# Kernel optimization log

Measured on AMD Instinct MI355X. Metric: run time of the kernel, lower is better.

## Reference

```python
import jax, jax.numpy as jnp
import numpy as np

B, N, M, DIM, H, DH = 2, 2048, 2048, 512, 8, 64
INNER = H * DH
SCALE = DH ** -0.5  # cosine_sim=False default
EPS = 1e-5


def layer_norm(x, g, b):
    mu = x.mean(-1, keepdims=True)
    var = ((x - mu) ** 2).mean(-1, keepdims=True)
    return (x - mu) * jax.lax.rsqrt(var + EPS) * g + b


def setup_inputs() -> dict:
    key = jax.random.key(0)
    ks = jax.random.split(key, 8)
    x = jax.random.normal(ks[0], (B, N, DIM), dtype=jnp.float32)
    context = jax.random.normal(ks[1], (B, M, DIM), dtype=jnp.float32)
    mask = jax.random.randint(ks[2], (B, M), 0, 2).astype(bool)
    Wq = jax.random.normal(ks[3], (DIM, INNER), dtype=jnp.float32) * 0.02
    Wkv = jax.random.normal(ks[4], (DIM, 2 * INNER), dtype=jnp.float32) * 0.02
    Wo = jax.random.normal(ks[5], (INNER, DIM), dtype=jnp.float32) * 0.02
    ln_g = jnp.ones((DIM,), jnp.float32)
    ln_b = jnp.zeros((DIM,), jnp.float32)
    lno_g = jnp.ones((DIM,), jnp.float32)
    lno_b = jnp.zeros((DIM,), jnp.float32)
    return {"x": x, "context": context, "mask": mask, "ln_g": ln_g, "ln_b": ln_b,
            "Wq": Wq, "Wkv": Wkv, "Wo": Wo, "lno_g": lno_g, "lno_b": lno_b}


def reference(x, context, mask, ln_g, ln_b, Wq, Wkv, Wo, lno_g, lno_b):
    b, n, _ = x.shape
    xn = layer_norm(x, ln_g, ln_b)
    ctx = context  # norm_context=False -> Identity
    q = (xn @ Wq).reshape(b, n, H, DH).transpose(0, 2, 1, 3)          # b h n d
    kv = ctx @ Wkv
    k, v = jnp.split(kv, 2, axis=-1)
    k = k.reshape(b, -1, H, DH).transpose(0, 2, 1, 3)                 # b h m d
    v = v.reshape(b, -1, H, DH).transpose(0, 2, 1, 3)
    q = q * SCALE
    k = k * SCALE
    sim = jnp.einsum('bhid,bhjd->bhij', q, k)                         # b h n m (256 MB)
    max_neg = -jnp.finfo(sim.dtype).max
    sim = jnp.where(mask[:, None, None, :], sim, max_neg)
    attn = jax.nn.softmax(sim.astype(jnp.float32), axis=-1).astype(sim.dtype)
    out = jnp.einsum('bhij,bhjd->bhid', attn, v)
    out = out.transpose(0, 2, 1, 3).reshape(b, n, INNER)
    return layer_norm(out @ Wo, lno_g, lno_b)
```

## Files before the change

### kernel.cpp

```cpp
#include <hip/hip_runtime.h>
#include <stdint.h>

typedef float f32x4 __attribute__((ext_vector_type(4)));
typedef float f32x16 __attribute__((ext_vector_type(16)));
typedef __bf16 bf16x8 __attribute__((ext_vector_type(8)));
typedef unsigned int uint2v __attribute__((ext_vector_type(2)));

#define MFMA16(a,b,c) __builtin_amdgcn_mfma_f32_16x16x32_bf16((a),(b),(c),0,0,0)
#define MFMA32(a,b,c) __builtin_amdgcn_mfma_f32_32x32x16_bf16((a),(b),(c),0,0,0)

__device__ __forceinline__ unsigned short f2bf(float f){
  unsigned int u = __float_as_uint(f);
  u += 0x7FFFu + ((u >> 16) & 1u);
  return (unsigned short)(u >> 16);
}

__device__ __forceinline__ unsigned cvtpk(float lo, float hi){
  unsigned r;
  asm volatile("v_cvt_pk_bf16_f32 %0, %1, %2" : "=v"(r) : "v"(lo), "v"(hi));
  return r;
}

__device__ __forceinline__ float fexp2(float x){
#if __has_builtin(__builtin_amdgcn_exp2f)
  return __builtin_amdgcn_exp2f(x);
#else
  return exp2f(x);
#endif
}

__device__ __forceinline__ void plswap(unsigned &a, unsigned &b){
#if __has_builtin(__builtin_amdgcn_permlane32_swap)
  uint2v r = __builtin_amdgcn_permlane32_swap(a, b, false, false);
  a = r[0]; b = r[1];
#else
  unsigned xa = __shfl_xor(a, 32), xb = __shfl_xor(b, 32);
  int hi = (threadIdx.x & 63) >> 5;
  unsigned na = hi ? xb : a;
  unsigned nb = hi ? b : xa;
  a = na; b = nb;
#endif
}

__device__ __forceinline__ float xpair_max(float x){
  unsigned a = __float_as_uint(x), b = a;
  plswap(a, b);
  return fmaxf(__uint_as_float(a), __uint_as_float(b));
}
__device__ __forceinline__ float xpair_sum(float x){
  unsigned a = __float_as_uint(x), b = a;
  plswap(a, b);
  return __uint_as_float(a) + __uint_as_float(b);
}

__device__ __forceinline__ void stage16(const unsigned short* g, unsigned short* l){
  __builtin_amdgcn_global_load_lds(
      (const __attribute__((address_space(1))) void*)g,
      (__attribute__((address_space(3))) void*)l, 16, 0, 0);
}

__global__ __launch_bounds__(256) void k_prep(
    const float* __restrict__ Wq, const float* __restrict__ Wkv, const float* __restrict__ Wo,
    const float* __restrict__ x, const float* __restrict__ ln_g, const float* __restrict__ ln_b,
    const float* __restrict__ ctx, const int* __restrict__ mask,
    unsigned short* __restrict__ WqT, unsigned short* __restrict__ WkvT, unsigned short* __restrict__ WoT,
    unsigned short* __restrict__ xn, unsigned short* __restrict__ cb, unsigned int* __restrict__ mb)
{
  __shared__ float tile[32][33];
  const int bid = blockIdx.x, t = threadIdx.x;
  if (bid < 1024) {
    const float* W; unsigned short* WT; int N, bx, by;
    if (bid < 256)      { W = Wq;  WT = WqT;  N = 512;  bx = bid & 15;        by = bid >> 4; }
    else if (bid < 768) { W = Wkv; WT = WkvT; N = 1024; bx = (bid-256) & 31;  by = (bid-256) >> 5; }
    else                { W = Wo;  WT = WoT;  N = 512;  bx = (bid-768) & 15;  by = (bid-768) >> 4; }
    const int tx = t & 31, ty = t >> 5;
    #pragma unroll
    for (int i = 0; i < 4; i++)
      tile[ty + i*8][tx] = W[(size_t)(by*32 + ty + i*8) * N + bx*32 + tx];
    __syncthreads();
    #pragma unroll
    for (int i = 0; i < 4; i++)
      WT[(size_t)(bx*32 + ty + i*8) * 512 + by*32 + tx] = f2bf(tile[tx][ty + i*8]);
  } else if (bid < 2048) {
    int row = (bid - 1024) * 4 + (t >> 6);
    int lane = t & 63;
    const float4* xr = (const float4*)(x + (size_t)row * 512);
    float4 a = xr[lane], c = xr[64 + lane];
    float s = a.x + a.y + a.z + a.w + c.x + c.y + c.z + c.w;
    #pragma unroll
    for (int o = 32; o; o >>= 1) s += __shfl_xor(s, o);
    float mu = s * (1.0f / 512.0f);
    float va = (a.x-mu)*(a.x-mu) + (a.y-mu)*(a.y-mu) + (a.z-mu)*(a.z-mu) + (a.w-mu)*(a.w-mu)
             + (c.x-mu)*(c.x-mu) + (c.y-mu)*(c.y-mu) + (c.z-mu)*(c.z-mu) + (c.w-mu)*(c.w-mu);
    #pragma unroll
    for (int o = 32; o; o >>= 1) va += __shfl_xor(va, o);
    float inv = rsqrtf(va * (1.0f / 512.0f) + 1e-5f);
    const float4* gp = (const float4*)ln_g;
    const float4* bp = (const float4*)ln_b;
    float4 g0 = gp[lane], g1 = gp[64 + lane], b0 = bp[lane], b1 = bp[64 + lane];
    ushort4* op = (ushort4*)(xn + (size_t)row * 512);
    op[lane]      = make_ushort4(f2bf((a.x-mu)*inv*g0.x + b0.x), f2bf((a.y-mu)*inv*g0.y + b0.y),
                                 f2bf((a.z-mu)*inv*g0.z + b0.z), f2bf((a.w-mu)*inv*g0.w + b0.w));
    op[64 + lane] = make_ushort4(f2bf((c.x-mu)*inv*g1.x + b1.x), f2bf((c.y-mu)*inv*g1.y + b1.y),
                                 f2bf((c.z-mu)*inv*g1.z + b1.z), f2bf((c.w-mu)*inv*g1.w + b1.w));
  } else if (bid < 4096) {
    int i = (bid - 2048) * 256 + t;
    float4 v = ((const float4*)ctx)[i];
    ((ushort4*)cb)[i] = make_ushort4(f2bf(v.x), f2bf(v.y), f2bf(v.z), f2bf(v.w));
  } else {
    int g = (bid - 4096) * 4 + (t >> 6);
    int ln = t & 63;
    int v = mask[g * 64 + ln];
    unsigned long long bb = __ballot(v != 0);
    if (ln == 0) { mb[g*2] = (unsigned)bb; mb[g*2+1] = (unsigned)(bb >> 32); }
  }
}

__global__ __launch_bounds__(256) void k_layernorm_f(
    const float* __restrict__ X, const float* __restrict__ G,
    const float* __restrict__ Bt, float* __restrict__ out)
{
  int row = blockIdx.x * 4 + (threadIdx.x >> 6);
  int lane = threadIdx.x & 63;
  const float4* xr = (const float4*)(X + (size_t)row * 512);
  float4 a = xr[lane], c = xr[64 + lane];
  float s = a.x + a.y + a.z + a.w + c.x + c.y + c.z + c.w;
  #pragma unroll
  for (int o = 32; o; o >>= 1) s += __shfl_xor(s, o);
  float mu = s * (1.0f / 512.0f);
  float va = (a.x-mu)*(a.x-mu) + (a.y-mu)*(a.y-mu) + (a.z-mu)*(a.z-mu) + (a.w-mu)*(a.w-mu)
           + (c.x-mu)*(c.x-mu) + (c.y-mu)*(c.y-mu) + (c.z-mu)*(c.z-mu) + (c.w-mu)*(c.w-mu);
  #pragma unroll
  for (int o = 32; o; o >>= 1) va += __shfl_xor(va, o);
  float inv = rsqrtf(va * (1.0f / 512.0f) + 1e-5f);
  const float4* gp = (const float4*)G;
  const float4* bp = (const float4*)Bt;
  float4 g0 = gp[lane], g1 = gp[64 + lane], b0 = bp[lane], b1 = bp[64 + lane];
  float4 y0, y1;
  y0.x = (a.x-mu)*inv*g0.x + b0.x; y0.y = (a.y-mu)*inv*g0.y + b0.y;
  y0.z = (a.z-mu)*inv*g0.z + b0.z; y0.w = (a.w-mu)*inv*g0.w + b0.w;
  y1.x = (c.x-mu)*inv*g1.x + b1.x; y1.y = (c.y-mu)*inv*g1.y + b1.y;
  y1.z = (c.z-mu)*inv*g1.z + b1.z; y1.w = (c.w-mu)*inv*g1.w + b1.w;
  float4* op = (float4*)(out + (size_t)row * 512);
  op[lane] = y0; op[64 + lane] = y1;
}

template<int MODE>
__device__ __forceinline__ void gemm_body(
    const unsigned short* __restrict__ A, const unsigned short* __restrict__ BT,
    void* __restrict__ out0, void* __restrict__ out1, int bx, int by,
    unsigned short* smem)
{
  unsigned short* As = smem;
  unsigned short* Bs = smem + 2*64*64;
  const int t = threadIdx.x;
  const int lane = t & 63, l16 = lane & 15, lhi = lane >> 4;
  const int w = t >> 6, wm = w >> 1, wn = w & 1;
  const int rowBase = by * 64;
  const int colBase = bx * 128;
  const int srr = lane >> 3, scw = lane & 7;

  f32x4 acc[2][4];
  #pragma unroll
  for (int i = 0; i < 2; i++)
    #pragma unroll
    for (int j = 0; j < 4; j++)
      acc[i][j] = f32x4{0.f, 0.f, 0.f, 0.f};

  auto STAGE = [&](int buf, int kt) {
    unsigned short* Ab = As + buf * 4096;
    unsigned short* Bb = Bs + buf * 8192;
    #pragma unroll
    for (int i = 0; i < 2; i++) {
      int rr = i * 32 + w * 8 + srr;
      stage16(A + (size_t)(rowBase + rr) * 512 + kt * 64 + ((scw ^ (rr & 7)) * 8),
              Ab + (i * 32 + w * 8) * 64);
    }
    #pragma unroll
    for (int i = 0; i < 4; i++) {
      int rr = i * 32 + w * 8 + srr;
      stage16(BT + (size_t)(colBase + rr) * 512 + kt * 64 + ((scw ^ (rr & 7)) * 8),
              Bb + (i * 32 + w * 8) * 64);
    }
  };

  STAGE(0, 0);
  __syncthreads();
  for (int kt = 0; kt < 8; ++kt) {
    const int buf = kt & 1;
    if (kt < 7) STAGE(buf ^ 1, kt + 1);
    const char* Ab = (const char*)(As + buf * 4096);
    const char* Bb = (const char*)(Bs + buf * 8192);
    #pragma unroll
    for (int ks = 0; ks < 2; ++ks) {
      bf16x8 af[2], bb[4];
      #pragma unroll
      for (int mi = 0; mi < 2; mi++) {
        int rr = wm * 32 + mi * 16 + l16;
        int cc = ks * 4 + lhi;
        af[mi] = *(const bf16x8*)(Ab + rr * 128 + ((cc ^ (rr & 7)) * 16));
      }
      #pragma unroll
      for (int ni = 0; ni < 4; ni++) {
        int rr = wn * 64 + ni * 16 + l16;
        int cc = ks * 4 + lhi;
        bb[ni] = *(const bf16x8*)(Bb + rr * 128 + ((cc ^ (rr & 7)) * 16));
      }
      #pragma unroll
      for (int mi = 0; mi < 2; mi++)
        #pragma unroll
        for (int ni = 0; ni < 4; ni++)
          acc[mi][ni] = MFMA16(af[mi], bb[ni], acc[mi][ni]);
    }
    __syncthreads();
  }

  if constexpr (MODE == 2) {
    const int r0 = rowBase + wm * 32 + lhi * 4;
    const int c0 = colBase + wn * 64 + l16;
    #pragma unroll
    for (int mi = 0; mi < 2; mi++)
      #pragma unroll
      for (int ni = 0; ni < 4; ni++)
        #pragma unroll
        for (int r = 0; r < 4; r++)
          ((float*)out0)[(size_t)(r0 + mi * 16 + r) * 512 + c0 + ni * 16] = acc[mi][ni][r];
  } else {
    unsigned short* stg = smem;
    const bool isV = (MODE == 1) && (colBase >= 512);
    if (!isV) {
      #pragma unroll
      for (int mi = 0; mi < 2; mi++) {
        int rl = wm * 32 + mi * 16 + lhi * 4;
        int tl = rl >> 5;
        #pragma unroll
        for (int ni = 0; ni < 4; ni++) {
          int cl = wn * 64 + ni * 16 + l16;
          int hl = cl >> 6, d = cl & 63;
          int rbase = (hl * 2 + tl) * 2048 + (d >> 4) * 512 + 256 * ((d >> 3) & 1) + (d & 7);
          #pragma unroll
          for (int r = 0; r < 4; r++)
            stg[rbase + ((rl + r) & 31) * 8] = f2bf(acc[mi][ni][r]);
        }
      }
    } else {
      #pragma unroll
      for (int mi = 0; mi < 2; mi++) {
        int rl = wm * 32 + mi * 16 + lhi * 4;
        int tl = rl >> 5, kvr = rl & 31;
        #pragma unroll
        for (int ni = 0; ni < 4; ni++) {
          int cl = wn * 64 + ni * 16 + l16;
          int hl = cl >> 6, d = cl & 63;
          int off = (hl * 2 + tl) * 2048 + (d >> 5) * 1024 + ((kvr >> 4) & 1) * 512
                  + ((d & 31) + 32 * ((kvr >> 3) & 1)) * 8 + (kvr & 7);
          ushort4 p = make_ushort4(f2bf(acc[mi][ni][0]), f2bf(acc[mi][ni][1]),
                                   f2bf(acc[mi][ni][2]), f2bf(acc[mi][ni][3]));
          *(ushort4*)(stg + off) = p;
        }
      }
    }
    __syncthreads();
    const int bb2 = rowBase >> 11;
    const int hh0 = (colBase & 511) >> 6;
    const int tile0 = (rowBase & 2047) >> 5;
    unsigned short* gout = (unsigned short*)(isV ? out1 : out0);
    #pragma unroll
    for (int ridx = 0; ridx < 4; ridx++) {
      int hl = ridx >> 1, tl = ridx & 1;
      size_t gb = ((size_t)((bb2 * 8 + hh0 + hl) * 64 + tile0 + tl)) * 2048 + t * 8;
      *(uint4*)(gout + gb) = *(const uint4*)(stg + ridx * 2048 + t * 8);
    }
  }
}

__global__ __launch_bounds__(256, 2) void k_qkv(
    const unsigned short* __restrict__ xn, const unsigned short* __restrict__ WqT,
    unsigned short* __restrict__ Qp,
    const unsigned short* __restrict__ cb, const unsigned short* __restrict__ WkvT,
    unsigned short* __restrict__ Kp, unsigned short* __restrict__ Vp)
{
  __shared__ __align__(16) unsigned short smem[2*64*64 + 2*128*64];
  const int bid = blockIdx.x;
  const int xcd = bid & 7, loc = bid >> 3;
  const int mloc = loc / 12, ct = loc % 12;
  const int mtile = xcd * 8 + mloc;
  if (ct < 4) gemm_body<0>(xn, WqT, Qp, nullptr, ct, mtile, smem);
  else        gemm_body<1>(cb, WkvT, Kp, Vp, ct - 4, mtile, smem);
}

__global__ __launch_bounds__(256, 2) void k_oproj(
    const unsigned short* __restrict__ ao, const unsigned short* __restrict__ WoT,
    float* __restrict__ proj)
{
  __shared__ __align__(16) unsigned short smem[2*64*64 + 2*128*64];
  const int bid = blockIdx.x;
  const int xcd = bid & 7, loc = bid >> 3;
  const int mloc = loc >> 2, ct = loc & 3;
  const int mtile = xcd * 8 + mloc;
  gemm_body<2>(ao, WoT, proj, nullptr, ct, mtile, smem);
}

__global__ __launch_bounds__(256, 3) void k_attn(
    const unsigned short* __restrict__ Qp, const unsigned short* __restrict__ Kp,
    const unsigned short* __restrict__ Vp, const unsigned int* __restrict__ mb,
    unsigned short* __restrict__ O)
{
  __shared__ __align__(16) float mbuf[3][64][34];
  const int t = threadIdx.x, lane = t & 63, q5 = lane & 31, hi = lane >> 5;
  const int w = t >> 6;
  const int bid = blockIdx.x;
  const int bh = (bid & 7) * 2 + (bid >> 9);
  const int qt = (bid >> 3) & 63;
  const int q0 = qt * 32;
  const int b = bh >> 3, h = bh & 7;
  const float C2f = 0.022542110013890053f;

  bf16x8 qf[4];
  {
    const unsigned short* qp = Qp + (size_t)(bh * 64 + qt) * 2048 + lane * 8;
    #pragma unroll
    for (int kk = 0; kk < 4; kk++) qf[kk] = *(const bf16x8*)(qp + kk * 512);
  }
  const unsigned short* kpb = Kp + (size_t)bh * 131072 + lane * 8;
  const unsigned short* vpb = Vp + (size_t)bh * 131072 + lane * 8;
  const unsigned int* mbp = mb + b * 64;

  float mrun = -3e38f, lrun = 0.f;
  f32x16 acc0, acc1;
  #pragma unroll
  for (int i = 0; i < 16; i++) { acc0[i] = 0.f; acc1[i] = 0.f; }

  bf16x8 kf[4], vf[4];
  auto loadK = [&](int tile) {
    #pragma unroll
    for (int kk = 0; kk < 4; kk++)
      kf[kk] = *(const bf16x8*)(kpb + (size_t)tile * 2048 + kk * 512);
  };
  auto loadV = [&](int tile) {
    #pragma unroll
    for (int i = 0; i < 4; i++)
      vf[i] = *(const bf16x8*)(vpb + (size_t)tile * 2048 + i * 512);
  };

  const int tb = w * 16;
  loadK(tb); loadV(tb);
  for (int it = 0; it < 16; ++it) {
    const int ti = tb + it;

    f32x16 s;
    #pragma unroll
    for (int i = 0; i < 16; i++) s[i] = 0.f;
    __builtin_amdgcn_s_setprio(1);
    #pragma unroll
    for (int kk = 0; kk < 4; kk++) s = MFMA32(kf[kk], qf[kk], s);
    __builtin_amdgcn_s_setprio(0);
    if (it < 15) loadK(ti + 1);

    float m0 = fmaxf(fmaxf(s[0], s[1]),  fmaxf(s[2], s[3]));
    float m1 = fmaxf(fmaxf(s[4], s[5]),  fmaxf(s[6], s[7]));
    float m2 = fmaxf(fmaxf(s[8], s[9]),  fmaxf(s[10], s[11]));
    float m3 = fmaxf(fmaxf(s[12], s[13]), fmaxf(s[14], s[15]));
    float tmax = fmaxf(fmaxf(m0, m1), fmaxf(m2, m3));
    tmax = xpair_max(tmax);
    if (!__all(tmax <= mrun + 400.f)) {
      float mnew = fmaxf(mrun, tmax);
      float sf = fexp2((mrun - mnew) * C2f);
      lrun *= sf;
      #pragma unroll
      for (int i = 0; i < 16; i++) { acc0[i] *= sf; acc1[i] *= sf; }
      mrun = mnew;
    }
    unsigned mh = mbp[ti] >> (hi * 4);
    float nb = -mrun * C2f;
    float p[16];
    #pragma unroll
    for (int r = 0; r < 16; r++) {
      float pv = fexp2(fmaf(s[r], C2f, nb));
      p[r] = ((mh >> ((r & 3) + 8 * (r >> 2))) & 1u) ? pv : 0.f;
    }
    float rsa = (p[0] + p[1]) + (p[2] + p[3]);
    float rsb = (p[4] + p[5]) + (p[6] + p[7]);
    float rsc = (p[8] + p[9]) + (p[10] + p[11]);
    float rsd = (p[12] + p[13]) + (p[14] + p[15]);
    lrun += (rsa + rsb) + (rsc + rsd);

    unsigned wd[8];
    #pragma unroll
    for (int i = 0; i < 8; i++) wd[i] = cvtpk(p[2 * i], p[2 * i + 1]);
    plswap(wd[0], wd[2]); plswap(wd[1], wd[3]);
    plswap(wd[4], wd[6]); plswap(wd[5], wd[7]);
    union { unsigned u[4]; bf16x8 v; } U0, U1;
    U0.u[0] = wd[0]; U0.u[1] = wd[1]; U0.u[2] = wd[2]; U0.u[3] = wd[3];
    U1.u[0] = wd[4]; U1.u[1] = wd[5]; U1.u[2] = wd[6]; U1.u[3] = wd[7];

    __builtin_amdgcn_s_setprio(1);
    acc0 = MFMA32(vf[0], U0.v, acc0);
    acc0 = MFMA32(vf[1], U1.v, acc0);
    acc1 = MFMA32(vf[2], U0.v, acc1);
    acc1 = MFMA32(vf[3], U1.v, acc1);
    __builtin_amdgcn_s_setprio(0);
    if (it < 15) loadV(ti + 1);
  }

  if (w) {
    #pragma unroll
    for (int i = 0; i < 16; i++) { mbuf[w-1][lane][i] = acc0[i]; mbuf[w-1][lane][16 + i] = acc1[i]; }
    mbuf[w-1][lane][32] = mrun; mbuf[w-1][lane][33] = lrun;
  }
  __syncthreads();
  if (!w) {
    float mo[3], lo[3];
    #pragma unroll
    for (int wv = 0; wv < 3; wv++) { mo[wv] = mbuf[wv][lane][32]; lo[wv] = mbuf[wv][lane][33]; }
    float mN = fmaxf(fmaxf(mrun, mo[0]), fmaxf(mo[1], mo[2]));
    float sf0 = fexp2((mrun - mN) * C2f);
    float sfv[3];
    float lsum = lrun * sf0;
    #pragma unroll
    for (int wv = 0; wv < 3; wv++) { sfv[wv] = fexp2((mo[wv] - mN) * C2f); lsum += lo[wv] * sfv[wv]; }
    lsum = xpair_sum(lsum);
    float linv = 1.f / lsum;
    float a2[32];
    #pragma unroll
    for (int i = 0; i < 16; i++) {
      float v0 = acc0[i] * sf0, v1 = acc1[i] * sf0;
      #pragma unroll
      for (int wv = 0; wv < 3; wv++) {
        v0 += mbuf[wv][lane][i] * sfv[wv];
        v1 += mbuf[wv][lane][16 + i] * sfv[wv];
      }
      a2[i] = v0 * linv;
      a2[16 + i] = v1 * linv;
    }
    unsigned short* ot = (unsigned short*)&mbuf[0][0][0];
    #pragma unroll
    for (int d2 = 0; d2 < 2; d2++)
      #pragma unroll
      for (int i = 0; i < 8; i++) {
        int d0 = ((2 * i) & 3) + 8 * (i >> 1) + 4 * hi + 32 * d2;
        unsigned wv2 = cvtpk(a2[d2 * 16 + 2 * i], a2[d2 * 16 + 2 * i + 1]);
        *(unsigned*)(ot + q5 * 72 + d0) = wv2;
      }
    #pragma unroll
    for (int it2 = 0; it2 < 4; ++it2) {
      int row = (lane >> 3) + it2 * 8, ch = lane & 7;
      uint4 val = *(const uint4*)(ot + row * 72 + ch * 8);
      *(uint4*)(O + ((size_t)(b * 2048 + q0 + row)) * 512 + h * 64 + ch * 8) = val;
    }
  }
}

extern "C" void kernel_launch(void* const* d_in, const int* in_sizes, int n_in,
                              void* d_out, int out_size, void* d_ws, size_t ws_size,
                              hipStream_t stream) {
  const float* x     = (const float*)d_in[0];
  const float* ctx   = (const float*)d_in[1];
  const int*   mask  = (const int*)d_in[2];
  const float* ln_g  = (const float*)d_in[3];
  const float* ln_b  = (const float*)d_in[4];
  const float* Wq    = (const float*)d_in[5];
  const float* Wkv   = (const float*)d_in[6];
  const float* Wo    = (const float*)d_in[7];
  const float* lno_g = (const float*)d_in[8];
  const float* lno_b = (const float*)d_in[9];
  float* out = (float*)d_out;

  char* ws = (char*)d_ws;
  unsigned short* WqT  = (unsigned short*)(ws + 0);
  unsigned short* WkvT = (unsigned short*)(ws + (size_t)1 * (1 << 19));
  unsigned short* WoT  = (unsigned short*)(ws + (size_t)3 * (1 << 19));
  unsigned short* xn   = (unsigned short*)(ws + (size_t)2  * (1 << 20));
  unsigned short* cb   = (unsigned short*)(ws + (size_t)6  * (1 << 20));
  unsigned short* Qp   = (unsigned short*)(ws + (size_t)10 * (1 << 20));
  unsigned short* Kp   = (unsigned short*)(ws + (size_t)14 * (1 << 20));
  unsigned short* Vp   = (unsigned short*)(ws + (size_t)18 * (1 << 20));
  unsigned short* ao   = (unsigned short*)(ws + (size_t)22 * (1 << 20));
  float* proj          = (float*)(ws + (size_t)26 * (1 << 20));
  unsigned int* mbw    = (unsigned int*)(ws + (size_t)26 * (1 << 20));

  k_prep<<<4112, 256, 0, stream>>>(Wq, Wkv, Wo, x, ln_g, ln_b, ctx, mask,
                                   WqT, WkvT, WoT, xn, cb, mbw);
  k_qkv<<<768, 256, 0, stream>>>(xn, WqT, Qp, cb, WkvT, Kp, Vp);
  k_attn<<<1024, 256, 0, stream>>>(Qp, Kp, Vp, mbw, ao);
  k_oproj<<<256, 256, 0, stream>>>(ao, WoT, proj);
  k_layernorm_f<<<1024, 256, 0, stream>>>(proj, lno_g, lno_b, out);
}
```

Measured before the change: 63.23 us.

## Process two query tiles per attention block to reuse K/V fragment loads

Each attention block now handles two 32-row query tiles that share every K and V fragment loaded per iteration, which halves global K/V traffic per query and halves the grid to 512 blocks. Launch bounds drop from 3 to 2 blocks per SM because of the doubled accumulators and Q registers. The cost is lower occupancy, less latency hiding, and a second merge pass with extra barriers at the end.

```diff
diff --git a/kernel.cpp b/kernel.cpp
--- a/kernel.cpp
+++ b/kernel.cpp
@@ -301,7 +301,7 @@
   gemm_body<2>(ao, WoT, proj, nullptr, ct, mtile, smem);
 }
 
-__global__ __launch_bounds__(256, 3) void k_attn(
+__global__ __launch_bounds__(256, 2) void k_attn(
     const unsigned short* __restrict__ Qp, const unsigned short* __restrict__ Kp,
     const unsigned short* __restrict__ Vp, const unsigned int* __restrict__ mb,
     unsigned short* __restrict__ O)
@@ -310,26 +310,29 @@
   const int t = threadIdx.x, lane = t & 63, q5 = lane & 31, hi = lane >> 5;
   const int w = t >> 6;
   const int bid = blockIdx.x;
-  const int bh = (bid & 7) * 2 + (bid >> 9);
-  const int qt = (bid >> 3) & 63;
-  const int q0 = qt * 32;
+  const int bh = (bid & 7) * 2 + (bid >> 8);
+  const int g = (bid >> 3) & 31;
+  const int qtA = g * 2, qtB = g * 2 + 1;
   const int b = bh >> 3, h = bh & 7;
   const float C2f = 0.022542110013890053f;
 
-  bf16x8 qf[4];
+  bf16x8 qfA[4], qfB[4];
   {
-    const unsigned short* qp = Qp + (size_t)(bh * 64 + qt) * 2048 + lane * 8;
-    #pragma unroll
-    for (int kk = 0; kk < 4; kk++) qf[kk] = *(const bf16x8*)(qp + kk * 512);
+    const unsigned short* qpA = Qp + (size_t)(bh * 64 + qtA) * 2048 + lane * 8;
+    const unsigned short* qpB = Qp + (size_t)(bh * 64 + qtB) * 2048 + lane * 8;
+    #pragma unroll
+    for (int kk = 0; kk < 4; kk++) { qfA[kk] = *(const bf16x8*)(qpA + kk * 512);
+                                     qfB[kk] = *(const bf16x8*)(qpB + kk * 512); }
   }
   const unsigned short* kpb = Kp + (size_t)bh * 131072 + lane * 8;
   const unsigned short* vpb = Vp + (size_t)bh * 131072 + lane * 8;
   const unsigned int* mbp = mb + b * 64;
 
-  float mrun = -3e38f, lrun = 0.f;
-  f32x16 acc0, acc1;
+  float mrunA = -3e38f, lrunA = 0.f;
+  float mrunB = -3e38f, lrunB = 0.f;
+  f32x16 accA0, accA1, accB0, accB1;
   #pragma unroll
-  for (int i = 0; i < 16; i++) { acc0[i] = 0.f; acc1[i] = 0.f; }
+  for (int i = 0; i < 16; i++) { accA0[i] = 0.f; accA1[i] = 0.f; accB0[i] = 0.f; accB1[i] = 0.f; }
 
   bf16x8 kf[4], vf[4];
   auto loadK = [&](int tile) {
@@ -343,24 +346,12 @@
       vf[i] = *(const bf16x8*)(vpb + (size_t)tile * 2048 + i * 512);
   };
 
-  const int tb = w * 16;
-  loadK(tb); loadV(tb);
-  for (int it = 0; it < 16; ++it) {
-    const int ti = tb + it;
-
-    f32x16 s;
-    #pragma unroll
-    for (int i = 0; i < 16; i++) s[i] = 0.f;
-    __builtin_amdgcn_s_setprio(1);
-    #pragma unroll
-    for (int kk = 0; kk < 4; kk++) s = MFMA32(kf[kk], qf[kk], s);
-    __builtin_amdgcn_s_setprio(0);
-    if (it < 15) loadK(ti + 1);
-
-    float m0 = fmaxf(fmaxf(s[0], s[1]),  fmaxf(s[2], s[3]));
-    float m1 = fmaxf(fmaxf(s[4], s[5]),  fmaxf(s[6], s[7]));
-    float m2 = fmaxf(fmaxf(s[8], s[9]),  fmaxf(s[10], s[11]));
-    float m3 = fmaxf(fmaxf(s[12], s[13]), fmaxf(s[14], s[15]));
+  auto smax_pv = [&](f32x16& sX, float& mrun, float& lrun, f32x16& a0, f32x16& a1,
+                     unsigned mh) {
+    float m0 = fmaxf(fmaxf(sX[0], sX[1]),  fmaxf(sX[2], sX[3]));
+    float m1 = fmaxf(fmaxf(sX[4], sX[5]),  fmaxf(sX[6], sX[7]));
+    float m2 = fmaxf(fmaxf(sX[8], sX[9]),  fmaxf(sX[10], sX[11]));
+    float m3 = fmaxf(fmaxf(sX[12], sX[13]), fmaxf(sX[14], sX[15]));
     float tmax = fmaxf(fmaxf(m0, m1), fmaxf(m2, m3));
     tmax = xpair_max(tmax);
     if (!__all(tmax <= mrun + 400.f)) {
@@ -368,15 +359,14 @@
       float sf = fexp2((mrun - mnew) * C2f);
       lrun *= sf;
       #pragma unroll
-      for (int i = 0; i < 16; i++) { acc0[i] *= sf; acc1[i] *= sf; }
+      for (int i = 0; i < 16; i++) { a0[i] *= sf; a1[i] *= sf; }
       mrun = mnew;
     }
-    unsigned mh = mbp[ti] >> (hi * 4);
     float nb = -mrun * C2f;
     float p[16];
     #pragma unroll
     for (int r = 0; r < 16; r++) {
-      float pv = fexp2(fmaf(s[r], C2f, nb));
+      float pv = fexp2(fmaf(sX[r], C2f, nb));
       p[r] = ((mh >> ((r & 3) + 8 * (r >> 2))) & 1u) ? pv : 0.f;
     }
     float rsa = (p[0] + p[1]) + (p[2] + p[3]);
@@ -395,60 +385,86 @@
     U1.u[0] = wd[4]; U1.u[1] = wd[5]; U1.u[2] = wd[6]; U1.u[3] = wd[7];
 
     __builtin_amdgcn_s_setprio(1);
-    acc0 = MFMA32(vf[0], U0.v, acc0);
-    acc0 = MFMA32(vf[1], U1.v, acc0);
-    acc1 = MFMA32(vf[2], U0.v, acc1);
-    acc1 = MFMA32(vf[3], U1.v, acc1);
+    a0 = MFMA32(vf[0], U0.v, a0);
+    a0 = MFMA32(vf[1], U1.v, a0);
+    a1 = MFMA32(vf[2], U0.v, a1);
+    a1 = MFMA32(vf[3], U1.v, a1);
     __builtin_amdgcn_s_setprio(0);
+  };
+
+  const int tb = w * 16;
+  loadK(tb); loadV(tb);
+  for (int it = 0; it < 16; ++it) {
+    const int ti = tb + it;
+
+    f32x16 sA, sB;
+    #pragma unroll
+    for (int i = 0; i < 16; i++) { sA[i] = 0.f; sB[i] = 0.f; }
+    __builtin_amdgcn_s_setprio(1);
+    #pragma unroll
+    for (int kk = 0; kk < 4; kk++) sA = MFMA32(kf[kk], qfA[kk], sA);
+    #pragma unroll
+    for (int kk = 0; kk < 4; kk++) sB = MFMA32(kf[kk], qfB[kk], sB);
+    __builtin_amdgcn_s_setprio(0);
+    if (it < 15) loadK(ti + 1);
+
+    unsigned mh = mbp[ti] >> (hi * 4);
+    smax_pv(sA, mrunA, lrunA, accA0, accA1, mh);
+    smax_pv(sB, mrunB, lrunB, accB0, accB1, mh);
     if (it < 15) loadV(ti + 1);
   }
 
-  if (w) {
-    #pragma unroll
-    for (int i = 0; i < 16; i++) { mbuf[w-1][lane][i] = acc0[i]; mbuf[w-1][lane][16 + i] = acc1[i]; }
-    mbuf[w-1][lane][32] = mrun; mbuf[w-1][lane][33] = lrun;
-  }
-  __syncthreads();
-  if (!w) {
-    float mo[3], lo[3];
-    #pragma unroll
-    for (int wv = 0; wv < 3; wv++) { mo[wv] = mbuf[wv][lane][32]; lo[wv] = mbuf[wv][lane][33]; }
-    float mN = fmaxf(fmaxf(mrun, mo[0]), fmaxf(mo[1], mo[2]));
-    float sf0 = fexp2((mrun - mN) * C2f);
-    float sfv[3];
-    float lsum = lrun * sf0;
-    #pragma unroll
-    for (int wv = 0; wv < 3; wv++) { sfv[wv] = fexp2((mo[wv] - mN) * C2f); lsum += lo[wv] * sfv[wv]; }
-    lsum = xpair_sum(lsum);
-    float linv = 1.f / lsum;
-    float a2[32];
-    #pragma unroll
-    for (int i = 0; i < 16; i++) {
-      float v0 = acc0[i] * sf0, v1 = acc1[i] * sf0;
-      #pragma unroll
-      for (int wv = 0; wv < 3; wv++) {
-        v0 += mbuf[wv][lane][i] * sfv[wv];
-        v1 += mbuf[wv][lane][16 + i] * sfv[wv];
+  auto merge_write = [&](f32x16& a0, f32x16& a1, float mr, float lr, int qt) {
+    if (w) {
+      #pragma unroll
+      for (int i = 0; i < 16; i++) { mbuf[w-1][lane][i] = a0[i]; mbuf[w-1][lane][16 + i] = a1[i]; }
+      mbuf[w-1][lane][32] = mr; mbuf[w-1][lane][33] = lr;
+    }
+    __syncthreads();
+    if (!w) {
+      float mo[3], lo[3];
+      #pragma unroll
+      for (int wv = 0; wv < 3; wv++) { mo[wv] = mbuf[wv][lane][32]; lo[wv] = mbuf[wv][lane][33]; }
+      float mN = fmaxf(fmaxf(mr, mo[0]), fmaxf(mo[1], mo[2]));
+      float sf0 = fexp2((mr - mN) * C2f);
+      float sfv[3];
+      float lsum = lr * sf0;
+      #pragma unroll
+      for (int wv = 0; wv < 3; wv++) { sfv[wv] = fexp2((mo[wv] - mN) * C2f); lsum += lo[wv] * sfv[wv]; }
+      lsum = xpair_sum(lsum);
+      float linv = 1.f / lsum;
+      float a2[32];
+      #pragma unroll
+      for (int i = 0; i < 16; i++) {
+        float v0 = a0[i] * sf0, v1 = a1[i] * sf0;
+        #pragma unroll
+        for (int wv = 0; wv < 3; wv++) {
+          v0 += mbuf[wv][lane][i] * sfv[wv];
+          v1 += mbuf[wv][lane][16 + i] * sfv[wv];
+        }
+        a2[i] = v0 * linv;
+        a2[16 + i] = v1 * linv;
       }
-      a2[i] = v0 * linv;
-      a2[16 + i] = v1 * linv;
-    }
-    unsigned short* ot = (unsigned short*)&mbuf[0][0][0];
-    #pragma unroll
-    for (int d2 = 0; d2 < 2; d2++)
-      #pragma unroll
-      for (int i = 0; i < 8; i++) {
-        int d0 = ((2 * i) & 3) + 8 * (i >> 1) + 4 * hi + 32 * d2;
-        unsigned wv2 = cvtpk(a2[d2 * 16 + 2 * i], a2[d2 * 16 + 2 * i + 1]);
-        *(unsigned*)(ot + q5 * 72 + d0) = wv2;
+      unsigned short* ot = (unsigned short*)&mbuf[0][0][0];
+      #pragma unroll
+      for (int d2 = 0; d2 < 2; d2++)
+        #pragma unroll
+        for (int i = 0; i < 8; i++) {
+          int d0 = ((2 * i) & 3) + 8 * (i >> 1) + 4 * hi + 32 * d2;
+          unsigned wv2 = cvtpk(a2[d2 * 16 + 2 * i], a2[d2 * 16 + 2 * i + 1]);
+          *(unsigned*)(ot + q5 * 72 + d0) = wv2;
+        }
+      #pragma unroll
+      for (int it2 = 0; it2 < 4; ++it2) {
+        int row = (lane >> 3) + it2 * 8, ch = lane & 7;
+        uint4 val = *(const uint4*)(ot + row * 72 + ch * 8);
+        *(uint4*)(O + ((size_t)(b * 2048 + qt * 32 + row)) * 512 + h * 64 + ch * 8) = val;
       }
-    #pragma unroll
-    for (int it2 = 0; it2 < 4; ++it2) {
-      int row = (lane >> 3) + it2 * 8, ch = lane & 7;
-      uint4 val = *(const uint4*)(ot + row * 72 + ch * 8);
-      *(uint4*)(O + ((size_t)(b * 2048 + q0 + row)) * 512 + h * 64 + ch * 8) = val;
-    }
-  }
+    }
+    __syncthreads();
+  };
+  merge_write(accA0, accA1, mrunA, lrunA, qtA);
+  merge_write(accB0, accB1, mrunB, lrunB, qtB);
 }
 
 extern "C" void kernel_launch(void* const* d_in, const int* in_sizes, int n_in,
@@ -482,7 +498,7 @@
   k_prep<<<4112, 256, 0, stream>>>(Wq, Wkv, Wo, x, ln_g, ln_b, ctx, mask,
                                    WqT, WkvT, WoT, xn, cb, mbw);
   k_qkv<<<768, 256, 0, stream>>>(xn, WqT, Qp, cb, WkvT, Kp, Vp);
-  k_attn<<<1024, 256, 0, stream>>>(Qp, Kp, Vp, mbw, ao);
+  k_attn<<<512, 256, 0, stream>>>(Qp, Kp, Vp, mbw, ao);
   k_oproj<<<256, 256, 0, stream>>>(ao, WoT, proj);
   k_layernorm_f<<<1024, 256, 0, stream>>>(proj, lno_g, lno_b, out);
 }
```

Measured after the change: 61.68 us. -2.4%, faster.

## Fold key mask into an MFMA bias and pair two KV tiles per iteration

Applied to the files above, without the earlier changes.

The key mask becomes an additive bf16 bias tensor in k_prep. It is applied by one extra MFMA per KV tile, using a one-hot Q fragment, instead of per-element bit tests and selects after exp. Each attention block now covers two query tiles, with two waves per query tile splitting the keys. Each wave handles two KV tiles per loop iteration, which doubles registers and the work per wave, while the grid is halved and launch bounds drop to 2. The intent is to remove mask ALU work and shrink the cross-wave merge, at the cost of fewer resident waves for latency hiding and higher register pressure.

```diff
diff --git a/kernel.cpp b/kernel.cpp
--- a/kernel.cpp
+++ b/kernel.cpp
@@ -64,7 +64,7 @@
     const float* __restrict__ x, const float* __restrict__ ln_g, const float* __restrict__ ln_b,
     const float* __restrict__ ctx, const int* __restrict__ mask,
     unsigned short* __restrict__ WqT, unsigned short* __restrict__ WkvT, unsigned short* __restrict__ WoT,
-    unsigned short* __restrict__ xn, unsigned short* __restrict__ cb, unsigned int* __restrict__ mb)
+    unsigned short* __restrict__ xn, unsigned short* __restrict__ cb, unsigned short* __restrict__ kbias)
 {
   __shared__ float tile[32][33];
   const int bid = blockIdx.x, t = threadIdx.x;
@@ -108,11 +108,16 @@
     float4 v = ((const float4*)ctx)[i];
     ((ushort4*)cb)[i] = make_ushort4(f2bf(v.x), f2bf(v.y), f2bf(v.z), f2bf(v.w));
   } else {
-    int g = (bid - 4096) * 4 + (t >> 6);
-    int ln = t & 63;
-    int v = mask[g * 64 + ln];
-    unsigned long long bb = __ballot(v != 0);
-    if (ln == 0) { mb[g*2] = (unsigned)bb; mb[g*2+1] = (unsigned)(bb >> 32); }
+    int i = (bid - 4096) * 256 + t;
+    int b2 = i >> 11, kv = i & 2047;
+    int tl = kv >> 5, ln = kv & 31;
+    unsigned short bias = (mask[b2 * 2048 + kv] != 0) ? (unsigned short)0 : f2bf(-1e6f);
+    ushort4* p0 = (ushort4*)(kbias + ((size_t)((b2 * 64 + tl) * 64 + ln)) * 8);
+    p0[0] = make_ushort4(bias, 0, 0, 0);
+    p0[1] = make_ushort4(0, 0, 0, 0);
+    ushort4* p1 = (ushort4*)(kbias + ((size_t)((b2 * 64 + tl) * 64 + ln + 32)) * 8);
+    p1[0] = make_ushort4(0, 0, 0, 0);
+    p1[1] = make_ushort4(0, 0, 0, 0);
   }
 }
 
@@ -301,18 +306,18 @@
   gemm_body<2>(ao, WoT, proj, nullptr, ct, mtile, smem);
 }
 
-__global__ __launch_bounds__(256, 3) void k_attn(
+__global__ __launch_bounds__(256, 2) void k_attn(
     const unsigned short* __restrict__ Qp, const unsigned short* __restrict__ Kp,
-    const unsigned short* __restrict__ Vp, const unsigned int* __restrict__ mb,
+    const unsigned short* __restrict__ Vp, const unsigned short* __restrict__ KB,
     unsigned short* __restrict__ O)
 {
-  __shared__ __align__(16) float mbuf[3][64][34];
+  __shared__ __align__(16) float mbuf[2][64][34];
   const int t = threadIdx.x, lane = t & 63, q5 = lane & 31, hi = lane >> 5;
-  const int w = t >> 6;
+  const int w = t >> 6, pr = w >> 1, half = w & 1;
   const int bid = blockIdx.x;
-  const int bh = (bid & 7) * 2 + (bid >> 9);
-  const int qt = (bid >> 3) & 63;
-  const int q0 = qt * 32;
+  const int bh = (bid & 7) * 2 + (bid >> 8);
+  const int g = (bid >> 3) & 31;
+  const int qt = g * 2 + pr;
   const int b = bh >> 3, h = bh & 7;
   const float C2f = 0.022542110013890053f;
 
@@ -324,44 +329,63 @@
   }
   const unsigned short* kpb = Kp + (size_t)bh * 131072 + lane * 8;
   const unsigned short* vpb = Vp + (size_t)bh * 131072 + lane * 8;
-  const unsigned int* mbp = mb + b * 64;
+  const unsigned short* kbb = KB + (size_t)b * 32768 + lane * 8;
+
+  union { unsigned u[4]; bf16x8 v; } QB;
+  QB.u[0] = (lane < 32) ? 0x00003F80u : 0u;
+  QB.u[1] = 0u; QB.u[2] = 0u; QB.u[3] = 0u;
+  f32x16 zv;
+  #pragma unroll
+  for (int i = 0; i < 16; i++) zv[i] = 0.f;
 
   float mrun = -3e38f, lrun = 0.f;
   f32x16 acc0, acc1;
   #pragma unroll
   for (int i = 0; i < 16; i++) { acc0[i] = 0.f; acc1[i] = 0.f; }
 
-  bf16x8 kf[4], vf[4];
+  bf16x8 kf[8], vf[8], kbf[2];
   auto loadK = [&](int tile) {
     #pragma unroll
-    for (int kk = 0; kk < 4; kk++)
-      kf[kk] = *(const bf16x8*)(kpb + (size_t)tile * 2048 + kk * 512);
+    for (int kk = 0; kk < 4; kk++) {
+      kf[kk]     = *(const bf16x8*)(kpb + (size_t)tile * 2048 + kk * 512);
+      kf[4 + kk] = *(const bf16x8*)(kpb + (size_t)(tile + 1) * 2048 + kk * 512);
+    }
+    kbf[0] = *(const bf16x8*)(kbb + (size_t)tile * 512);
+    kbf[1] = *(const bf16x8*)(kbb + (size_t)(tile + 1) * 512);
   };
   auto loadV = [&](int tile) {
     #pragma unroll
-    for (int i = 0; i < 4; i++)
-      vf[i] = *(const bf16x8*)(vpb + (size_t)tile * 2048 + i * 512);
+    for (int i = 0; i < 4; i++) {
+      vf[i]     = *(const bf16x8*)(vpb + (size_t)tile * 2048 + i * 512);
+      vf[4 + i] = *(const bf16x8*)(vpb + (size_t)(tile + 1) * 2048 + i * 512);
+    }
   };
 
-  const int tb = w * 16;
+  const int tb = half * 32;
   loadK(tb); loadV(tb);
   for (int it = 0; it < 16; ++it) {
-    const int ti = tb + it;
-
-    f32x16 s;
-    #pragma unroll
-    for (int i = 0; i < 16; i++) s[i] = 0.f;
+    const int ti = tb + it * 2;
+
     __builtin_amdgcn_s_setprio(1);
-    #pragma unroll
-    for (int kk = 0; kk < 4; kk++) s = MFMA32(kf[kk], qf[kk], s);
+    f32x16 sL = MFMA32(kbf[0], QB.v, zv);
+    f32x16 sH = MFMA32(kbf[1], QB.v, zv);
+    #pragma unroll
+    for (int kk = 0; kk < 4; kk++) sL = MFMA32(kf[kk], qf[kk], sL);
+    #pragma unroll
+    for (int kk = 0; kk < 4; kk++) sH = MFMA32(kf[4 + kk], qf[kk], sH);
     __builtin_amdgcn_s_setprio(0);
-    if (it < 15) loadK(ti + 1);
-
-    float m0 = fmaxf(fmaxf(s[0], s[1]),  fmaxf(s[2], s[3]));
-    float m1 = fmaxf(fmaxf(s[4], s[5]),  fmaxf(s[6], s[7]));
-    float m2 = fmaxf(fmaxf(s[8], s[9]),  fmaxf(s[10], s[11]));
-    float m3 = fmaxf(fmaxf(s[12], s[13]), fmaxf(s[14], s[15]));
-    float tmax = fmaxf(fmaxf(m0, m1), fmaxf(m2, m3));
+    if (it < 15) loadK(ti + 2);
+
+    float a0 = fmaxf(fmaxf(sL[0], sL[1]),  fmaxf(sL[2], sL[3]));
+    float a1 = fmaxf(fmaxf(sL[4], sL[5]),  fmaxf(sL[6], sL[7]));
+    float a2 = fmaxf(fmaxf(sL[8], sL[9]),  fmaxf(sL[10], sL[11]));
+    float a3 = fmaxf(fmaxf(sL[12], sL[13]), fmaxf(sL[14], sL[15]));
+    float b0 = fmaxf(fmaxf(sH[0], sH[1]),  fmaxf(sH[2], sH[3]));
+    float b1 = fmaxf(fmaxf(sH[4], sH[5]),  fmaxf(sH[6], sH[7]));
+    float b2 = fmaxf(fmaxf(sH[8], sH[9]),  fmaxf(sH[10], sH[11]));
+    float b3 = fmaxf(fmaxf(sH[12], sH[13]), fmaxf(sH[14], sH[15]));
+    float tmax = fmaxf(fmaxf(fmaxf(a0, a1), fmaxf(a2, a3)),
+                       fmaxf(fmaxf(b0, b1), fmaxf(b2, b3)));
     tmax = xpair_max(tmax);
     if (!__all(tmax <= mrun + 400.f)) {
       float mnew = fmaxf(mrun, tmax);
@@ -371,69 +395,64 @@
       for (int i = 0; i < 16; i++) { acc0[i] *= sf; acc1[i] *= sf; }
       mrun = mnew;
     }
-    unsigned mh = mbp[ti] >> (hi * 4);
     float nb = -mrun * C2f;
-    float p[16];
-    #pragma unroll
-    for (int r = 0; r < 16; r++) {
-      float pv = fexp2(fmaf(s[r], C2f, nb));
-      p[r] = ((mh >> ((r & 3) + 8 * (r >> 2))) & 1u) ? pv : 0.f;
-    }
-    float rsa = (p[0] + p[1]) + (p[2] + p[3]);
-    float rsb = (p[4] + p[5]) + (p[6] + p[7]);
-    float rsc = (p[8] + p[9]) + (p[10] + p[11]);
-    float rsd = (p[12] + p[13]) + (p[14] + p[15]);
-    lrun += (rsa + rsb) + (rsc + rsd);
-
-    unsigned wd[8];
-    #pragma unroll
-    for (int i = 0; i < 8; i++) wd[i] = cvtpk(p[2 * i], p[2 * i + 1]);
-    plswap(wd[0], wd[2]); plswap(wd[1], wd[3]);
-    plswap(wd[4], wd[6]); plswap(wd[5], wd[7]);
-    union { unsigned u[4]; bf16x8 v; } U0, U1;
-    U0.u[0] = wd[0]; U0.u[1] = wd[1]; U0.u[2] = wd[2]; U0.u[3] = wd[3];
-    U1.u[0] = wd[4]; U1.u[1] = wd[5]; U1.u[2] = wd[6]; U1.u[3] = wd[7];
+    #pragma unroll
+    for (int r = 0; r < 16; r++) sL[r] = fexp2(fmaf(sL[r], C2f, nb));
+    #pragma unroll
+    for (int r = 0; r < 16; r++) sH[r] = fexp2(fmaf(sH[r], C2f, nb));
+    lrun += (((sL[0]+sL[1])+(sL[2]+sL[3])) + ((sL[4]+sL[5])+(sL[6]+sL[7])))
+          + (((sL[8]+sL[9])+(sL[10]+sL[11])) + ((sL[12]+sL[13])+(sL[14]+sL[15])))
+          + (((sH[0]+sH[1])+(sH[2]+sH[3])) + ((sH[4]+sH[5])+(sH[6]+sH[7])))
+          + (((sH[8]+sH[9])+(sH[10]+sH[11])) + ((sH[12]+sH[13])+(sH[14]+sH[15])));
+
+    unsigned wa[8], wb[8];
+    #pragma unroll
+    for (int i = 0; i < 8; i++) { wa[i] = cvtpk(sL[2*i], sL[2*i+1]);
+                                  wb[i] = cvtpk(sH[2*i], sH[2*i+1]); }
+    plswap(wa[0], wa[2]); plswap(wa[1], wa[3]);
+    plswap(wa[4], wa[6]); plswap(wa[5], wa[7]);
+    plswap(wb[0], wb[2]); plswap(wb[1], wb[3]);
+    plswap(wb[4], wb[6]); plswap(wb[5], wb[7]);
+    union { unsigned u[4]; bf16x8 v; } UL0, UL1, UH0, UH1;
+    UL0.u[0]=wa[0]; UL0.u[1]=wa[1]; UL0.u[2]=wa[2]; UL0.u[3]=wa[3];
+    UL1.u[0]=wa[4]; UL1.u[1]=wa[5]; UL1.u[2]=wa[6]; UL1.u[3]=wa[7];
+    UH0.u[0]=wb[0]; UH0.u[1]=wb[1]; UH0.u[2]=wb[2]; UH0.u[3]=wb[3];
+    UH1.u[0]=wb[4]; UH1.u[1]=wb[5]; UH1.u[2]=wb[6]; UH1.u[3]=wb[7];
 
     __builtin_amdgcn_s_setprio(1);
-    acc0 = MFMA32(vf[0], U0.v, acc0);
-    acc0 = MFMA32(vf[1], U1.v, acc0);
-    acc1 = MFMA32(vf[2], U0.v, acc1);
-    acc1 = MFMA32(vf[3], U1.v, acc1);
+    acc0 = MFMA32(vf[0], UL0.v, acc0);
+    acc0 = MFMA32(vf[1], UL1.v, acc0);
+    acc1 = MFMA32(vf[2], UL0.v, acc1);
+    acc1 = MFMA32(vf[3], UL1.v, acc1);
+    acc0 = MFMA32(vf[4], UH0.v, acc0);
+    acc0 = MFMA32(vf[5], UH1.v, acc0);
+    acc1 = MFMA32(vf[6], UH0.v, acc1);
+    acc1 = MFMA32(vf[7], UH1.v, acc1);
     __builtin_amdgcn_s_setprio(0);
-    if (it < 15) loadV(ti + 1);
-  }
-
-  if (w) {
-    #pragma unroll
-    for (int i = 0; i < 16; i++) { mbuf[w-1][lane][i] = acc0[i]; mbuf[w-1][lane][16 + i] = acc1[i]; }
-    mbuf[w-1][lane][32] = mrun; mbuf[w-1][lane][33] = lrun;
+    if (it < 15) loadV(ti + 2);
+  }
+
+  if (half) {
+    #pragma unroll
+    for (int i = 0; i < 16; i++) { mbuf[pr][lane][i] = acc0[i]; mbuf[pr][lane][16 + i] = acc1[i]; }
+    mbuf[pr][lane][32] = mrun; mbuf[pr][lane][33] = lrun;
   }
   __syncthreads();
-  if (!w) {
-    float mo[3], lo[3];
-    #pragma unroll
-    for (int wv = 0; wv < 3; wv++) { mo[wv] = mbuf[wv][lane][32]; lo[wv] = mbuf[wv][lane][33]; }
-    float mN = fmaxf(fmaxf(mrun, mo[0]), fmaxf(mo[1], mo[2]));
+  if (!half) {
+    float m1 = mbuf[pr][lane][32], l1 = mbuf[pr][lane][33];
+    float mN = fmaxf(mrun, m1);
     float sf0 = fexp2((mrun - mN) * C2f);
-    float sfv[3];
-    float lsum = lrun * sf0;
-    #pragma unroll
-    for (int wv = 0; wv < 3; wv++) { sfv[wv] = fexp2((mo[wv] - mN) * C2f); lsum += lo[wv] * sfv[wv]; }
+    float sf1 = fexp2((m1 - mN) * C2f);
+    float lsum = lrun * sf0 + l1 * sf1;
     lsum = xpair_sum(lsum);
     float linv = 1.f / lsum;
     float a2[32];
     #pragma unroll
     for (int i = 0; i < 16; i++) {
-      float v0 = acc0[i] * sf0, v1 = acc1[i] * sf0;
-      #pragma unroll
-      for (int wv = 0; wv < 3; wv++) {
-        v0 += mbuf[wv][lane][i] * sfv[wv];
-        v1 += mbuf[wv][lane][16 + i] * sfv[wv];
-      }
-      a2[i] = v0 * linv;
-      a2[16 + i] = v1 * linv;
-    }
-    unsigned short* ot = (unsigned short*)&mbuf[0][0][0];
+      a2[i]      = (acc0[i] * sf0 + mbuf[pr][lane][i] * sf1) * linv;
+      a2[16 + i] = (acc1[i] * sf0 + mbuf[pr][lane][16 + i] * sf1) * linv;
+    }
+    unsigned short* ot = (unsigned short*)&mbuf[pr][0][0];
     #pragma unroll
     for (int d2 = 0; d2 < 2; d2++)
       #pragma unroll
@@ -446,7 +465,7 @@
     for (int it2 = 0; it2 < 4; ++it2) {
       int row = (lane >> 3) + it2 * 8, ch = lane & 7;
       uint4 val = *(const uint4*)(ot + row * 72 + ch * 8);
-      *(uint4*)(O + ((size_t)(b * 2048 + q0 + row)) * 512 + h * 64 + ch * 8) = val;
+      *(uint4*)(O + ((size_t)(b * 2048 + qt * 32 + row)) * 512 + h * 64 + ch * 8) = val;
     }
   }
 }
@@ -477,12 +496,12 @@
   unsigned short* Vp   = (unsigned short*)(ws + (size_t)18 * (1 << 20));
   unsigned short* ao   = (unsigned short*)(ws + (size_t)22 * (1 << 20));
   float* proj          = (float*)(ws + (size_t)26 * (1 << 20));
-  unsigned int* mbw    = (unsigned int*)(ws + (size_t)26 * (1 << 20));
+  unsigned short* kbias = (unsigned short*)(ws + (size_t)26 * (1 << 20));
 
   k_prep<<<4112, 256, 0, stream>>>(Wq, Wkv, Wo, x, ln_g, ln_b, ctx, mask,
-                                   WqT, WkvT, WoT, xn, cb, mbw);
+                                   WqT, WkvT, WoT, xn, cb, kbias);
   k_qkv<<<768, 256, 0, stream>>>(xn, WqT, Qp, cb, WkvT, Kp, Vp);
-  k_attn<<<1024, 256, 0, stream>>>(Qp, Kp, Vp, mbw, ao);
+  k_attn<<<512, 256, 0, stream>>>(Qp, Kp, Vp, kbias, ao);
   k_oproj<<<256, 256, 0, stream>>>(ao, WoT, proj);
   k_layernorm_f<<<1024, 256, 0, stream>>>(proj, lno_g, lno_b, out);
 }
```

Result: no change. 62.28 us (-1.5%).
